# Kernel optimization log

Measured on AMD Instinct MI355X. Metric: run time of the kernel, lower is better.

Reference implementation:

```python
import jax, jax.numpy as jnp
import numpy as np

N_NODES = 100000


def _gcn_edges(edge_index, num_nodes):
    # Add self-loops and compute symmetric GCN normalization per edge.
    src = jnp.concatenate([edge_index[0], jnp.arange(num_nodes, dtype=edge_index.dtype)])
    dst = jnp.concatenate([edge_index[1], jnp.arange(num_nodes, dtype=edge_index.dtype)])
    deg = jnp.zeros((num_nodes,), jnp.float32).at[dst].add(1.0)
    dinv = jnp.where(deg > 0, jax.lax.rsqrt(deg), 0.0)
    norm = dinv[src] * dinv[dst]  # [E+N]
    return src, dst, norm


def _gcn_conv(x, W, b, src, dst, norm, num_nodes):
    h = x @ W                         # [N, d_out] transform first (d_out <= d_in)
    msg = h[src] * norm[:, None]      # [E, d_out] gather + scale
    agg = jax.ops.segment_sum(msg, dst, num_segments=num_nodes)
    return agg + b


def setup_inputs() -> dict:
    key = jax.random.key(0)
    k = jax.random.split(key, 8)
    n, e, d_in, d_out = N_NODES, 1600000, 128, 64
    hid = 2 * d_out
    s = lambda fan: 1.0 / np.sqrt(fan)
    return {
        "x": jax.random.normal(k[0], (n, d_in), jnp.float32),
        "edge_index": jax.random.randint(k[1], (2, e), 0, n, jnp.int64),
        "W1": jax.random.normal(k[2], (d_in, hid), jnp.float32) * s(d_in),
        "b1": jnp.zeros((hid,), jnp.float32),
        "Wmu": jax.random.normal(k[3], (hid, d_out), jnp.float32) * s(hid),
        "bmu": jnp.zeros((d_out,), jnp.float32),
        "Wls": jax.random.normal(k[4], (hid, d_out), jnp.float32) * s(hid),
        "bls": jnp.zeros((d_out,), jnp.float32),
    }


def reference(x, edge_index, W1, b1, Wmu, bmu, Wls, bls):
    n = x.shape[0]
    src, dst, norm = _gcn_edges(edge_index, n)
    h = jax.nn.relu(_gcn_conv(x, W1, b1, src, dst, norm, n))
    mu = _gcn_conv(h, Wmu, bmu, src, dst, norm, n)
    logstd = _gcn_conv(h, Wls, bls, src, dst, norm, n)
    return mu, logstd
```

## Files before the change

kernel.cpp:

```cpp
#include <hip/hip_runtime.h>

#define DIN 128
#define HID 128
#define DOUT 64
#define NCHUNK 784
#define BSH 9
#define NB1MAX 256
#define BSLACK 1540

typedef unsigned short ushort_t;
typedef unsigned int uint_t;
typedef __attribute__((ext_vector_type(4))) short s4v;
typedef __attribute__((ext_vector_type(4))) float f4v;

#if defined(__has_builtin)
#if __has_builtin(__builtin_amdgcn_mfma_f32_16x16x16bf16_1k)
#define MFMA16(a, b, c) __builtin_amdgcn_mfma_f32_16x16x16bf16_1k(a, b, c, 0, 0, 0)
#endif
#endif
#ifndef MFMA16
static __device__ inline f4v mfma16_asm(s4v a, s4v b, f4v c) {
  asm volatile("v_mfma_f32_16x16x16_bf16 %0, %1, %2, %0" : "+v"(c) : "v"(a), "v"(b));
  return c;
}
#define MFMA16(a, b, c) mfma16_asm(a, b, c)
#endif

static inline int ceil_div(int a, int b) { return (a + b - 1) / b; }

__device__ inline ushort_t f2bf(float f) {
  uint_t u = __float_as_uint(f);
  u += 0x7fff + ((u >> 16) & 1);
  return (ushort_t)(u >> 16);
}
__device__ inline uint_t pack2bf(float a, float b) {
  return (uint_t)f2bf(a) | ((uint_t)f2bf(b) << 16);
}
__device__ inline float2 bf2x2(uint_t u) {
  return make_float2(__uint_as_float(u << 16), __uint_as_float(u & 0xffff0000u));
}

__device__ inline int blk_scan_incl(int v, int* ws, int nw) {
  int t = threadIdx.x, lane = t & 63, w = t >> 6;
#pragma unroll
  for (int d = 1; d < 64; d <<= 1) {
    int u = __shfl_up(v, d, 64);
    if (lane >= d) v += u;
  }
  if (lane == 63) ws[w] = v;
  __syncthreads();
  if (w == 0) {
    int s = (lane < nw) ? ws[lane] : 0;
    for (int d = 1; d < nw; d <<= 1) {
      int u = __shfl_up(s, d, 64);
      if (lane >= d) s += u;
    }
    if (lane < nw) ws[lane] = s;
  }
  __syncthreads();
  if (w > 0) v += ws[w - 1];
  return v;
}


__global__ __launch_bounds__(512) void k_setup(const int* __restrict__ dst, int E, int CH,
                                               int nb1, int* __restrict__ counts,
                                               const float* __restrict__ W1,
                                               const float* __restrict__ Wmu,
                                               const float* __restrict__ Wls,
                                               ushort_t* __restrict__ Wt1,
                                               ushort_t* __restrict__ Wt2,
                                               ushort_t* __restrict__ xWb,
                                               ushort_t* __restrict__ h,
                                               float* __restrict__ dinv, int N) {
  __shared__ uint_t cnt[NB1MAX];
  int b = blockIdx.x, t = threadIdx.x;
  if (b < NCHUNK) {
    for (int i = t; i < nb1; i += 512) cnt[i] = 0;
    __syncthreads();
    int e0 = b * CH, e1 = min(E, e0 + CH);
    for (int i = e0 + t; i < e1; i += 512) atomicAdd(&cnt[((uint_t)dst[i]) >> BSH], 1u);
    __syncthreads();
    for (int i = t; i < nb1; i += 512) counts[b * nb1 + i] = (int)cnt[i];
  } else if (b < NCHUNK + 32) {
    int idx = (b - NCHUNK) * 512 + t;
    int j = idx >> 7, k = idx & 127;
    Wt1[j * 128 + k] = f2bf(W1[k * 128 + j]);
    Wt2[j * 128 + k] = f2bf(j < 64 ? Wmu[k * 64 + j] : Wls[k * 64 + (j - 64)]);
  } else {
    if (t < 64) ((uint_t*)(xWb + (size_t)N * HID))[t] = 0;
    else if (t < 128) ((uint_t*)(h + (size_t)N * HID))[t - 64] = 0;
    else if (t == 128) dinv[N] = 0.f;
  }
}

__global__ __launch_bounds__(256) void k_bscan(const int* __restrict__ counts, int nb1,
                                               int* __restrict__ chunk_off,
                                               int* __restrict__ btot) {
  __shared__ int ws[8];
  __shared__ int shc;
  int b = blockIdx.x, t = threadIdx.x;
  int carry = 0;
#pragma unroll
  for (int r = 0; r < NCHUNK / 256 + 1; r++) {
    int idx = r * 256 + t;
    int v = (idx < NCHUNK) ? counts[idx * nb1 + b] : 0;
    int incl = blk_scan_incl(v, ws, 4) + carry;
    if (idx < NCHUNK) chunk_off[idx * nb1 + b] = incl - v;
    if (t == 255) shc = incl;
    __syncthreads();
    carry = shc;
  }
  if (t == 0) btot[b] = carry;
}

__global__ __launch_bounds__(256) void k_bscatter(const int* __restrict__ src,
                                                  const int* __restrict__ dst, int E, int CH,
                                                  int nb1, const int* __restrict__ btot,
                                                  const int* __restrict__ chunk_off,
                                                  uint_t* __restrict__ tmp) {
  __shared__ int ws[8];
  __shared__ uint_t cur[NB1MAX];
  int t = threadIdx.x, c = blockIdx.x;
  {
    int v = (t < nb1) ? btot[t] : 0;
    int incl = blk_scan_incl(v, ws, 4);
    if (t < nb1) cur[t] = (uint_t)(incl - v + chunk_off[c * nb1 + t]);
  }
  __syncthreads();
  int e0 = c * CH, e1 = min(E, e0 + CH);
  for (int i = e0 + t; i < e1; i += 256) {
    uint_t d = (uint_t)dst[i];
    uint_t s = (uint_t)src[i];
    uint_t p = atomicAdd(&cur[d >> BSH], 1u);
    tmp[p] = ((d & ((1u << BSH) - 1)) << 17) | s;
  }
}

__global__ __launch_bounds__(512) void k_bfinal(const uint_t* __restrict__ tmp,
                                                const int* __restrict__ btot, int N, int nb1,
                                                uint_t* __restrict__ csr,
                                                int* __restrict__ row_ptr,
                                                int* __restrict__ row_end,
                                                float* __restrict__ dinv) {
  __shared__ int ws[8];
  __shared__ int sseg0, sseg1;
  __shared__ uint_t cnt[1 << BSH];
  __shared__ uint_t ppfx[1 << BSH];
  __shared__ uint_t cur[1 << BSH];
  int b = blockIdx.x, t = threadIdx.x;
  {
    int v = (t < nb1) ? btot[t] : 0;
    int incl = blk_scan_incl(v, ws, 8);
    if (t == b) {
      sseg0 = incl - v;
      sseg1 = incl;
    }
  }
  for (int i = t; i < (1 << BSH); i += 512) cnt[i] = 0;
  __syncthreads();
  int seg0 = sseg0, seg1 = sseg1;
  int pb = ((seg0 + 3) & ~3) + BSLACK * b;
  for (int i = seg0 + t; i < seg1; i += 512) atomicAdd(&cnt[tmp[i] >> 17], 1u);
  __syncthreads();
  if (t < 64) {
    uint_t pc[8];
    uint_t s = 0;
#pragma unroll
    for (int k = 0; k < 8; k++) {
      pc[k] = (cnt[t * 8 + k] + 3u) & ~3u;
      s += pc[k];
    }
    int incl = (int)s;
#pragma unroll
    for (int d = 1; d < 64; d <<= 1) {
      int u = __shfl_up(incl, d, 64);
      if (t >= d) incl += u;
    }
    uint_t excl = (uint_t)incl - s;
#pragma unroll
    for (int k = 0; k < 8; k++) {
      ppfx[t * 8 + k] = excl;
      excl += pc[k];
    }
  }
  __syncthreads();
  int nd0 = b << BSH;
  for (int i = t; i < (1 << BSH); i += 512) {
    cur[i] = ppfx[i];
    int g = nd0 + i;
    if (g < N) {
      row_ptr[g] = pb + (int)ppfx[i];
      row_end[g] = pb + (int)(ppfx[i] + ((cnt[i] + 3u) & ~3u));
      dinv[g] = rsqrtf((float)cnt[i] + 1.0f);
    }
  }
  __syncthreads();
  for (int i = seg0 + t; i < seg1; i += 512) {
    uint_t v = tmp[i];
    uint_t pos = atomicAdd(&cur[v >> 17], 1u);
    csr[pb + (int)pos] = v & 0x1FFFFu;
  }
  __syncthreads();
  for (int i = t; i < (1 << BSH); i += 512) {
    uint_t e0 = cur[i];
    uint_t e1 = ppfx[i] + ((cnt[i] + 3u) & ~3u);
    for (uint_t k = e0; k < e1; k++) csr[pb + (int)k] = (uint_t)N;
  }
}


__global__ __launch_bounds__(256) void k_gemm1(const float* __restrict__ A,
                                               const ushort_t* __restrict__ Wt,
                                               const float* __restrict__ dinv,
                                               ushort_t* __restrict__ C, int n) {
  __shared__ ushort_t Ws[128][132];
  int t = threadIdx.x;
#pragma unroll
  for (int i = 0; i < 16; i++) {
    int f = t + 256 * i;
    int rowj = f >> 5, seg = f & 31;
    *(uint2*)&Ws[rowj][seg * 4] = *(const uint2*)(Wt + rowj * 128 + seg * 4);
  }
  __syncthreads();
  int w = t >> 6, lane = t & 63;
  int rl = lane & 15, g = lane >> 4;
  int row = blockIdx.x * 64 + w * 16 + rl;
  bool valid = row < n;
  const float* Ar = A + (size_t)row * DIN + 4 * g;
  s4v af[8];
#pragma unroll
  for (int kk = 0; kk < 8; kk++) {
    float4 v = make_float4(0.f, 0.f, 0.f, 0.f);
    if (valid) v = *(const float4*)(Ar + kk * 16);
    s4v a;
    a[0] = (short)f2bf(v.x);
    a[1] = (short)f2bf(v.y);
    a[2] = (short)f2bf(v.z);
    a[3] = (short)f2bf(v.w);
    af[kk] = a;
  }
  f4v acc[8];
#pragma unroll
  for (int ct = 0; ct < 8; ct++) acc[ct] = (f4v)0.f;
#pragma unroll
  for (int kk = 0; kk < 8; kk++) {
    int ko = kk * 16 + 4 * g;
#pragma unroll
    for (int ct = 0; ct < 8; ct++) {
      s4v b = *(s4v*)&Ws[ct * 16 + rl][ko];
      acc[ct] = MFMA16(af[kk], b, acc[ct]);
    }
  }
  int gr0 = blockIdx.x * 64 + w * 16 + 4 * g;
#pragma unroll
  for (int i = 0; i < 4; i++) {
    int gr = gr0 + i;
    if (gr < n) {
      float dv = dinv[gr];
#pragma unroll
      for (int ct = 0; ct < 8; ct++)
        C[(size_t)gr * HID + ct * 16 + rl] = f2bf(dv * acc[ct][i]);
    }
  }
}


__global__ __launch_bounds__(256) void k_agg(const ushort_t* __restrict__ H,
                                             const int* __restrict__ row_ptr,
                                             const int* __restrict__ row_end,
                                             const uint_t* __restrict__ csr,
                                             const float* __restrict__ dinv,
                                             const float* __restrict__ bias,
                                             ushort_t* __restrict__ out, int n,
                                             int prescale_relu) {
  int node = (blockIdx.x * blockDim.x + threadIdx.x) >> 6;
  int lane = threadIdx.x & 63;
  if (node >= n) return;
  const char* Hb = (const char*)H;
  uint_t loff = (uint_t)lane << 2;
  float dn = dinv[node];
  int j = row_ptr[node], end = row_end[node];
  float2 hs = bf2x2(*(const uint_t*)(Hb + ((size_t)(((uint_t)node << 8) | loff))));
  float ax = hs.x, ay = hs.y;
  if (j < end) {
    uint4 c = *(const uint4*)(csr + j);
    while (true) {
      int jn = j + 4;
      bool more = jn < end;
      uint4 cn;
      if (more) cn = *(const uint4*)(csr + jn);
      uint_t v0 = *(const uint_t*)(Hb + (size_t)((c.x << 8) | loff));
      uint_t v1 = *(const uint_t*)(Hb + (size_t)((c.y << 8) | loff));
      uint_t v2 = *(const uint_t*)(Hb + (size_t)((c.z << 8) | loff));
      uint_t v3 = *(const uint_t*)(Hb + (size_t)((c.w << 8) | loff));
      float2 f0 = bf2x2(v0), f1 = bf2x2(v1), f2 = bf2x2(v2), f3 = bf2x2(v3);
      ax += f0.x + f1.x;
      ay += f0.y + f1.y;
      ax += f2.x + f3.x;
      ay += f2.y + f3.y;
      if (!more) break;
      c = cn;
      j = jn;
    }
  }
  ax *= dn;
  ay *= dn;
  if (prescale_relu) {
    ax = fmaxf(ax + bias[2 * lane], 0.f) * dn;
    ay = fmaxf(ay + bias[2 * lane + 1], 0.f) * dn;
  }
  ((uint_t*)out)[(size_t)node * 64 + lane] = pack2bf(ax, ay);
}


__global__ __launch_bounds__(256) void k_gemm2(const ushort_t* __restrict__ A,
                                               const ushort_t* __restrict__ Wt,
                                               const float* __restrict__ bmu,
                                               const float* __restrict__ bls,
                                               float* __restrict__ out, int n) {
  __shared__ ushort_t Ws[128][132];
  int t = threadIdx.x;
#pragma unroll
  for (int i = 0; i < 16; i++) {
    int f = t + 256 * i;
    int rowj = f >> 5, seg = f & 31;
    *(uint2*)&Ws[rowj][seg * 4] = *(const uint2*)(Wt + rowj * 128 + seg * 4);
  }
  __syncthreads();
  int w = t >> 6, lane = t & 63;
  int rl = lane & 15, g = lane >> 4;
  int row = blockIdx.x * 64 + w * 16 + rl;
  bool valid = row < n;
  const ushort_t* Ar = A + (size_t)row * HID + 4 * g;
  s4v af[8];
#pragma unroll
  for (int kk = 0; kk < 8; kk++) {
    s4v a = (s4v)0;
    if (valid) a = *(const s4v*)(Ar + kk * 16);
    af[kk] = a;
  }
  f4v acc[8];
#pragma unroll
  for (int ct = 0; ct < 8; ct++) acc[ct] = (f4v)0.f;
#pragma unroll
  for (int kk = 0; kk < 8; kk++) {
    int ko = kk * 16 + 4 * g;
#pragma unroll
    for (int ct = 0; ct < 8; ct++) {
      s4v b = *(s4v*)&Ws[ct * 16 + rl][ko];
      acc[ct] = MFMA16(af[kk], b, acc[ct]);
    }
  }
  int gr0 = blockIdx.x * 64 + w * 16 + 4 * g;
#pragma unroll
  for (int ct = 0; ct < 8; ct++) {
    int col = ct * 16 + rl;
    float bv;
    size_t obase;
    int cc;
    if (ct < 4) {
      bv = bmu[col];
      obase = 0;
      cc = col;
    } else {
      bv = bls[col - 64];
      obase = (size_t)n * DOUT;
      cc = col - 64;
    }
#pragma unroll
    for (int i = 0; i < 4; i++) {
      int gr = gr0 + i;
      if (gr < n) out[obase + (size_t)gr * DOUT + cc] = acc[ct][i] + bv;
    }
  }
}


extern "C" void kernel_launch(void* const* d_in, const int* in_sizes, int n_in,
                              void* d_out, int out_size, void* d_ws, size_t ws_size,
                              hipStream_t stream) {
  const float* x   = (const float*)d_in[0];
  const int*   ei  = (const int*)d_in[1];
  const float* W1  = (const float*)d_in[2];
  const float* b1  = (const float*)d_in[3];
  const float* Wmu = (const float*)d_in[4];
  const float* bmu = (const float*)d_in[5];
  const float* Wls = (const float*)d_in[6];
  const float* bls = (const float*)d_in[7];
  float* out = (float*)d_out;

  const int N = in_sizes[0] / DIN;
  const int E = in_sizes[1] / 2;
  const int* esrc = ei;
  const int* edst = ei + E;
  const int nb1 = ceil_div(N, 1 << BSH);
  const int CH = ceil_div(E, NCHUNK);

  char* ws = (char*)d_ws;
  size_t off = 0;
  auto alloc = [&](size_t bytes) -> void* {
    void* p = ws + off;
    off = (off + bytes + 255) & ~(size_t)255;
    return p;
  };
  ushort_t* xWb   = (ushort_t*)alloc((size_t)(N + 1) * HID * sizeof(ushort_t));
  ushort_t* h     = (ushort_t*)alloc((size_t)(N + 1) * HID * sizeof(ushort_t));
  uint_t* csr     = (uint_t*)alloc(((size_t)E + (size_t)(BSLACK + 8) * nb1 + 16) * 4);
  uint_t* tmp     = (uint_t*)alloc((size_t)E * 4);
  int* counts     = (int*)alloc((size_t)NCHUNK * nb1 * 4);
  int* chunk_off  = (int*)alloc((size_t)NCHUNK * nb1 * 4);
  int* btot       = (int*)alloc((size_t)nb1 * 4);
  int* row_ptr    = (int*)alloc((size_t)N * 4);
  int* row_end    = (int*)alloc((size_t)N * 4);
  float* dinv     = (float*)alloc((size_t)(N + 1) * 4);
  ushort_t* wt1b  = (ushort_t*)alloc((size_t)HID * HID * 2);
  ushort_t* wt2b  = (ushort_t*)alloc((size_t)HID * HID * 2);
  (void)ws_size; (void)n_in; (void)out_size;

  k_setup<<<NCHUNK + 33, 512, 0, stream>>>(edst, E, CH, nb1, counts, W1, Wmu, Wls, wt1b, wt2b,
                                           xWb, h, dinv, N);
  k_bscan<<<nb1, 256, 0, stream>>>(counts, nb1, chunk_off, btot);
  k_bscatter<<<NCHUNK, 256, 0, stream>>>(esrc, edst, E, CH, nb1, btot, chunk_off, tmp);
  k_bfinal<<<nb1, 512, 0, stream>>>(tmp, btot, N, nb1, csr, row_ptr, row_end, dinv);

  k_gemm1<<<ceil_div(N, 64), 256, 0, stream>>>(x, wt1b, dinv, xWb, N);
  k_agg<<<ceil_div(N, 4), 256, 0, stream>>>(xWb, row_ptr, row_end, csr, dinv, b1, h, N, 1);

  k_agg<<<ceil_div(N, 4), 256, 0, stream>>>(h, row_ptr, row_end, csr, dinv, nullptr, xWb, N, 0);
  k_gemm2<<<ceil_div(N, 64), 256, 0, stream>>>(xWb, wt2b, bmu, bls, out, N);
}
```

Before: 216.5 us.

## Fuse GEMM1 into setup kernel and fuse second aggregation with GEMM2

The first dense transform X·W1 now runs inside the setup kernel, before the degrees are known. The source-side normalization therefore moves into the first aggregation as per-edge loads of dinv. The second aggregation is fused with the output GEMM: each 1024-thread block aggregates 16 nodes into shared memory and then runs MFMA against Wt2 read from global memory. This removes two kernel launches and the round trip of the aggregated intermediate through global memory. In exchange it adds an extra gather of dinv per edge in the first aggregation and a block-wide sync.

New measurement: 249.4 us. +15.2%, slower.

```diff
diff --git a/kernel.cpp b/kernel.cpp
--- a/kernel.cpp
+++ b/kernel.cpp
@@ -65,27 +65,77 @@
 
 __global__ __launch_bounds__(512) void k_setup(const int* __restrict__ dst, int E, int CH,
                                                int nb1, int* __restrict__ counts,
+                                               const float* __restrict__ x,
                                                const float* __restrict__ W1,
                                                const float* __restrict__ Wmu,
                                                const float* __restrict__ Wls,
-                                               ushort_t* __restrict__ Wt1,
                                                ushort_t* __restrict__ Wt2,
                                                ushort_t* __restrict__ xWb,
                                                ushort_t* __restrict__ h,
-                                               float* __restrict__ dinv, int N) {
+                                               float* __restrict__ dinv, int N, int G1) {
+  __shared__ ushort_t Ws[128][132];
   __shared__ uint_t cnt[NB1MAX];
   int b = blockIdx.x, t = threadIdx.x;
-  if (b < NCHUNK) {
+  if (b < G1) {
+#pragma unroll
+    for (int it = 0; it < 16; it++) {
+      int k = it * 8 + ((t >> 7) << 1);
+      int j = t & 127;
+      float a = W1[k * 128 + j];
+      float bb = W1[(k + 1) * 128 + j];
+      *(uint_t*)&Ws[j][k] = pack2bf(a, bb);
+    }
+    __syncthreads();
+    int w = t >> 6, lane = t & 63;
+    int rl = lane & 15, g = lane >> 4;
+    int row = b * 128 + w * 16 + rl;
+    bool valid = row < N;
+    const float* Ar = x + (size_t)row * DIN + 4 * g;
+    s4v af[8];
+#pragma unroll
+    for (int kk = 0; kk < 8; kk++) {
+      float4 v = make_float4(0.f, 0.f, 0.f, 0.f);
+      if (valid) v = *(const float4*)(Ar + kk * 16);
+      s4v a;
+      a[0] = (short)f2bf(v.x);
+      a[1] = (short)f2bf(v.y);
+      a[2] = (short)f2bf(v.z);
+      a[3] = (short)f2bf(v.w);
+      af[kk] = a;
+    }
+    f4v acc[8];
+#pragma unroll
+    for (int ct = 0; ct < 8; ct++) acc[ct] = (f4v)0.f;
+#pragma unroll
+    for (int kk = 0; kk < 8; kk++) {
+      int ko = kk * 16 + 4 * g;
+#pragma unroll
+      for (int ct = 0; ct < 8; ct++) {
+        s4v bb = *(s4v*)&Ws[ct * 16 + rl][ko];
+        acc[ct] = MFMA16(af[kk], bb, acc[ct]);
+      }
+    }
+    int gr0 = b * 128 + w * 16 + 4 * g;
+#pragma unroll
+    for (int i = 0; i < 4; i++) {
+      int gr = gr0 + i;
+      if (gr < N) {
+#pragma unroll
+        for (int ct = 0; ct < 8; ct++)
+          xWb[(size_t)gr * HID + ct * 16 + rl] = f2bf(acc[ct][i]);
+      }
+    }
+  } else if (b < G1 + NCHUNK) {
+    int c = b - G1;
     for (int i = t; i < nb1; i += 512) cnt[i] = 0;
     __syncthreads();
-    int e0 = b * CH, e1 = min(E, e0 + CH);
+    int e0 = c * CH, e1 = min(E, e0 + CH);
     for (int i = e0 + t; i < e1; i += 512) atomicAdd(&cnt[((uint_t)dst[i]) >> BSH], 1u);
     __syncthreads();
-    for (int i = t; i < nb1; i += 512) counts[b * nb1 + i] = (int)cnt[i];
-  } else if (b < NCHUNK + 32) {
-    int idx = (b - NCHUNK) * 512 + t;
+    for (int i = t; i < nb1; i += 512) counts[c * nb1 + i] = (int)cnt[i];
+  } else if (b < G1 + NCHUNK + 32) {
+    int idx = (b - G1 - NCHUNK) * 512 + t;
     int j = idx >> 7, k = idx & 127;
-    Wt1[j * 128 + k] = f2bf(W1[k * 128 + j]);
     Wt2[j * 128 + k] = f2bf(j < 64 ? Wmu[k * 64 + j] : Wls[k * 64 + (j - 64)]);
   } else {
     if (t < 64) ((uint_t*)(xWb + (size_t)N * HID))[t] = 0;
@@ -210,79 +260,23 @@
 }
 
 
-__global__ __launch_bounds__(256) void k_gemm1(const float* __restrict__ A,
-                                               const ushort_t* __restrict__ Wt,
-                                               const float* __restrict__ dinv,
-                                               ushort_t* __restrict__ C, int n) {
-  __shared__ ushort_t Ws[128][132];
-  int t = threadIdx.x;
-#pragma unroll
-  for (int i = 0; i < 16; i++) {
-    int f = t + 256 * i;
-    int rowj = f >> 5, seg = f & 31;
-    *(uint2*)&Ws[rowj][seg * 4] = *(const uint2*)(Wt + rowj * 128 + seg * 4);
-  }
-  __syncthreads();
-  int w = t >> 6, lane = t & 63;
-  int rl = lane & 15, g = lane >> 4;
-  int row = blockIdx.x * 64 + w * 16 + rl;
-  bool valid = row < n;
-  const float* Ar = A + (size_t)row * DIN + 4 * g;
-  s4v af[8];
-#pragma unroll
-  for (int kk = 0; kk < 8; kk++) {
-    float4 v = make_float4(0.f, 0.f, 0.f, 0.f);
-    if (valid) v = *(const float4*)(Ar + kk * 16);
-    s4v a;
-    a[0] = (short)f2bf(v.x);
-    a[1] = (short)f2bf(v.y);
-    a[2] = (short)f2bf(v.z);
-    a[3] = (short)f2bf(v.w);
-    af[kk] = a;
-  }
-  f4v acc[8];
-#pragma unroll
-  for (int ct = 0; ct < 8; ct++) acc[ct] = (f4v)0.f;
-#pragma unroll
-  for (int kk = 0; kk < 8; kk++) {
-    int ko = kk * 16 + 4 * g;
-#pragma unroll
-    for (int ct = 0; ct < 8; ct++) {
-      s4v b = *(s4v*)&Ws[ct * 16 + rl][ko];
-      acc[ct] = MFMA16(af[kk], b, acc[ct]);
-    }
-  }
-  int gr0 = blockIdx.x * 64 + w * 16 + 4 * g;
-#pragma unroll
-  for (int i = 0; i < 4; i++) {
-    int gr = gr0 + i;
-    if (gr < n) {
-      float dv = dinv[gr];
-#pragma unroll
-      for (int ct = 0; ct < 8; ct++)
-        C[(size_t)gr * HID + ct * 16 + rl] = f2bf(dv * acc[ct][i]);
-    }
-  }
-}
-
-
 __global__ __launch_bounds__(256) void k_agg(const ushort_t* __restrict__ H,
                                              const int* __restrict__ row_ptr,
                                              const int* __restrict__ row_end,
                                              const uint_t* __restrict__ csr,
                                              const float* __restrict__ dinv,
                                              const float* __restrict__ bias,
-                                             ushort_t* __restrict__ out, int n,
-                                             int prescale_relu) {
+                                             ushort_t* __restrict__ out, int n) {
   int node = (blockIdx.x * blockDim.x + threadIdx.x) >> 6;
   int lane = threadIdx.x & 63;
   if (node >= n) return;
   const char* Hb = (const char*)H;
+  const char* Db = (const char*)dinv;
   uint_t loff = (uint_t)lane << 2;
   float dn = dinv[node];
   int j = row_ptr[node], end = row_end[node];
   float2 hs = bf2x2(*(const uint_t*)(Hb + ((size_t)(((uint_t)node << 8) | loff))));
-  float ax = hs.x, ay = hs.y;
+  float ax = dn * hs.x, ay = dn * hs.y;
   if (j < end) {
     uint4 c = *(const uint4*)(csr + j);
     while (true) {
@@ -290,88 +284,94 @@
       bool more = jn < end;
       uint4 cn;
       if (more) cn = *(const uint4*)(csr + jn);
+      float w0 = *(const float*)(Db + (size_t)(c.x << 2));
+      float w1 = *(const float*)(Db + (size_t)(c.y << 2));
+      float w2 = *(const float*)(Db + (size_t)(c.z << 2));
+      float w3 = *(const float*)(Db + (size_t)(c.w << 2));
       uint_t v0 = *(const uint_t*)(Hb + (size_t)((c.x << 8) | loff));
       uint_t v1 = *(const uint_t*)(Hb + (size_t)((c.y << 8) | loff));
       uint_t v2 = *(const uint_t*)(Hb + (size_t)((c.z << 8) | loff));
       uint_t v3 = *(const uint_t*)(Hb + (size_t)((c.w << 8) | loff));
       float2 f0 = bf2x2(v0), f1 = bf2x2(v1), f2 = bf2x2(v2), f3 = bf2x2(v3);
-      ax += f0.x + f1.x;
-      ay += f0.y + f1.y;
-      ax += f2.x + f3.x;
-      ay += f2.y + f3.y;
+      ax += w0 * f0.x; ay += w0 * f0.y;
+      ax += w1 * f1.x; ay += w1 * f1.y;
+      ax += w2 * f2.x; ay += w2 * f2.y;
+      ax += w3 * f3.x; ay += w3 * f3.y;
       if (!more) break;
       c = cn;
       j = jn;
     }
   }
-  ax *= dn;
-  ay *= dn;
-  if (prescale_relu) {
-    ax = fmaxf(ax + bias[2 * lane], 0.f) * dn;
-    ay = fmaxf(ay + bias[2 * lane + 1], 0.f) * dn;
-  }
+  ax = fmaxf(dn * ax + bias[2 * lane], 0.f) * dn;
+  ay = fmaxf(dn * ay + bias[2 * lane + 1], 0.f) * dn;
   ((uint_t*)out)[(size_t)node * 64 + lane] = pack2bf(ax, ay);
 }
 
 
-__global__ __launch_bounds__(256) void k_gemm2(const ushort_t* __restrict__ A,
-                                               const ushort_t* __restrict__ Wt,
-                                               const float* __restrict__ bmu,
-                                               const float* __restrict__ bls,
-                                               float* __restrict__ out, int n) {
-  __shared__ ushort_t Ws[128][132];
-  int t = threadIdx.x;
-#pragma unroll
-  for (int i = 0; i < 16; i++) {
-    int f = t + 256 * i;
-    int rowj = f >> 5, seg = f & 31;
-    *(uint2*)&Ws[rowj][seg * 4] = *(const uint2*)(Wt + rowj * 128 + seg * 4);
-  }
-  __syncthreads();
-  int w = t >> 6, lane = t & 63;
-  int rl = lane & 15, g = lane >> 4;
-  int row = blockIdx.x * 64 + w * 16 + rl;
-  bool valid = row < n;
-  const ushort_t* Ar = A + (size_t)row * HID + 4 * g;
-  s4v af[8];
-#pragma unroll
-  for (int kk = 0; kk < 8; kk++) {
-    s4v a = (s4v)0;
-    if (valid) a = *(const s4v*)(Ar + kk * 16);
-    af[kk] = a;
-  }
-  f4v acc[8];
-#pragma unroll
-  for (int ct = 0; ct < 8; ct++) acc[ct] = (f4v)0.f;
-#pragma unroll
-  for (int kk = 0; kk < 8; kk++) {
-    int ko = kk * 16 + 4 * g;
-#pragma unroll
-    for (int ct = 0; ct < 8; ct++) {
-      s4v b = *(s4v*)&Ws[ct * 16 + rl][ko];
-      acc[ct] = MFMA16(af[kk], b, acc[ct]);
-    }
-  }
-  int gr0 = blockIdx.x * 64 + w * 16 + 4 * g;
-#pragma unroll
-  for (int ct = 0; ct < 8; ct++) {
+__global__ __launch_bounds__(1024) void k_agg2g(const ushort_t* __restrict__ H,
+                                                const int* __restrict__ row_ptr,
+                                                const int* __restrict__ row_end,
+                                                const uint_t* __restrict__ csr,
+                                                const float* __restrict__ dinv,
+                                                const ushort_t* __restrict__ Wt2,
+                                                const float* __restrict__ bmu,
+                                                const float* __restrict__ bls,
+                                                float* __restrict__ out, int n) {
+  __shared__ ushort_t rows[16][132];
+  int t = threadIdx.x, w = t >> 6, lane = t & 63;
+  int node = blockIdx.x * 16 + w;
+  float ax = 0.f, ay = 0.f;
+  if (node < n) {
+    const char* Hb = (const char*)H;
+    uint_t loff = (uint_t)lane << 2;
+    float dn = dinv[node];
+    int j = row_ptr[node], end = row_end[node];
+    float2 hs = bf2x2(*(const uint_t*)(Hb + ((size_t)(((uint_t)node << 8) | loff))));
+    ax = hs.x;
+    ay = hs.y;
+    if (j < end) {
+      uint4 c = *(const uint4*)(csr + j);
+      while (true) {
+        int jn = j + 4;
+        bool more = jn < end;
+        uint4 cn;
+        if (more) cn = *(const uint4*)(csr + jn);
+        uint_t v0 = *(const uint_t*)(Hb + (size_t)((c.x << 8) | loff));
+        uint_t v1 = *(const uint_t*)(Hb + (size_t)((c.y << 8) | loff));
+        uint_t v2 = *(const uint_t*)(Hb + (size_t)((c.z << 8) | loff));
+        uint_t v3 = *(const uint_t*)(Hb + (size_t)((c.w << 8) | loff));
+        float2 f0 = bf2x2(v0), f1 = bf2x2(v1), f2 = bf2x2(v2), f3 = bf2x2(v3);
+        ax += f0.x + f1.x;
+        ay += f0.y + f1.y;
+        ax += f2.x + f3.x;
+        ay += f2.y + f3.y;
+        if (!more) break;
+        c = cn;
+        j = jn;
+      }
+    }
+    ax *= dn;
+    ay *= dn;
+  }
+  *(uint_t*)&rows[w][2 * lane] = pack2bf(ax, ay);
+  __syncthreads();
+  if (w < 8) {
+    int ct = w, rl = lane & 15, g = lane >> 4;
+    f4v acc = (f4v)0.f;
+#pragma unroll
+    for (int kk = 0; kk < 8; kk++) {
+      s4v a = *(s4v*)&rows[rl][kk * 16 + 4 * g];
+      s4v b = *(const s4v*)(Wt2 + (size_t)(ct * 16 + rl) * 128 + kk * 16 + 4 * g);
+      acc = MFMA16(a, b, acc);
+    }
     int col = ct * 16 + rl;
-    float bv;
-    size_t obase;
-    int cc;
-    if (ct < 4) {
-      bv = bmu[col];
-      obase = 0;
-      cc = col;
-    } else {
-      bv = bls[col - 64];
-      obase = (size_t)n * DOUT;
-      cc = col - 64;
-    }
+    float bv = (col < 64) ? bmu[col] : bls[col - 64];
+    size_t obase = (col < 64) ? 0 : (size_t)n * DOUT;
+    int cc = col & 63;
 #pragma unroll
     for (int i = 0; i < 4; i++) {
-      int gr = gr0 + i;
-      if (gr < n) out[obase + (size_t)gr * DOUT + cc] = acc[ct][i] + bv;
+      int nd = blockIdx.x * 16 + 4 * g + i;
+      if (nd < n) out[obase + (size_t)nd * DOUT + cc] = acc[i] + bv;
     }
   }
 }
@@ -396,6 +396,7 @@
   const int* edst = ei + E;
   const int nb1 = ceil_div(N, 1 << BSH);
   const int CH = ceil_div(E, NCHUNK);
+  const int G1 = ceil_div(N, 128);
 
   char* ws = (char*)d_ws;
   size_t off = 0;
@@ -414,19 +415,17 @@
   int* row_ptr    = (int*)alloc((size_t)N * 4);
   int* row_end    = (int*)alloc((size_t)N * 4);
   float* dinv     = (float*)alloc((size_t)(N + 1) * 4);
-  ushort_t* wt1b  = (ushort_t*)alloc((size_t)HID * HID * 2);
   ushort_t* wt2b  = (ushort_t*)alloc((size_t)HID * HID * 2);
   (void)ws_size; (void)n_in; (void)out_size;
 
-  k_setup<<<NCHUNK + 33, 512, 0, stream>>>(edst, E, CH, nb1, counts, W1, Wmu, Wls, wt1b, wt2b,
-                                           xWb, h, dinv, N);
+  k_setup<<<G1 + NCHUNK + 33, 512, 0, stream>>>(edst, E, CH, nb1, counts, x, W1, Wmu, Wls,
+                                                wt2b, xWb, h, dinv, N, G1);
   k_bscan<<<nb1, 256, 0, stream>>>(counts, nb1, chunk_off, btot);
   k_bscatter<<<NCHUNK, 256, 0, stream>>>(esrc, edst, E, CH, nb1, btot, chunk_off, tmp);
   k_bfinal<<<nb1, 512, 0, stream>>>(tmp, btot, N, nb1, csr, row_ptr, row_end, dinv);
 
-  k_gemm1<<<ceil_div(N, 64), 256, 0, stream>>>(x, wt1b, dinv, xWb, N);
-  k_agg<<<ceil_div(N, 4), 256, 0, stream>>>(xWb, row_ptr, row_end, csr, dinv, b1, h, N, 1);
-
-  k_agg<<<ceil_div(N, 4), 256, 0, stream>>>(h, row_ptr, row_end, csr, dinv, nullptr, xWb, N, 0);
-  k_gemm2<<<ceil_div(N, 64), 256, 0, stream>>>(xWb, wt2b, bmu, bls, out, N);
-}
+  k_agg<<<ceil_div(N, 4), 256, 0, stream>>>(xWb, row_ptr, row_end, csr, dinv, b1, h, N);
+
+  k_agg2g<<<ceil_div(N, 16), 1024, 0, stream>>>(h, row_ptr, row_end, csr, dinv, wt2b, bmu, bls,
+                                                out, N);
+}
```
